# Kernel optimization log

Measured on AMD Instinct MI355X. Metric: run time of the kernel, lower is better.

## Reference

```python
import jax, jax.numpy as jnp
import numpy as np

N, IN_DIM, D, H, E, L = 50000, 16, 128, 256, 800000, 3


def setup_inputs() -> dict:
    key = jax.random.key(0)
    ks = jax.random.split(key, 32)
    s = 0.1
    inp = {
        "x": jax.random.normal(ks[0], (N, IN_DIM), dtype=jnp.float32),
        "edge_index": jax.random.randint(ks[1], (2, E), 0, N, dtype=jnp.int64),
        "enc_W": s * jax.random.normal(ks[2], (IN_DIM, D), dtype=jnp.float32),
        "enc_b": jnp.zeros((D,), jnp.float32),
        "msg_W1": s * jax.random.normal(ks[3], (L, 2 * D, H), dtype=jnp.float32),
        "msg_b1": jnp.zeros((L, H), jnp.float32),
        "msg_W2": s * jax.random.normal(ks[4], (L, H, H), dtype=jnp.float32),
        "msg_b2": jnp.zeros((L, H), jnp.float32),
        "msg_W3": s * jax.random.normal(ks[5], (L, H, D), dtype=jnp.float32),
        "msg_b3": jnp.zeros((L, D), jnp.float32),
        "gru_Wih": s * jax.random.normal(ks[6], (L, D, 3 * D), dtype=jnp.float32),
        "gru_Whh": s * jax.random.normal(ks[7], (L, D, 3 * D), dtype=jnp.float32),
        "gru_bih": jnp.zeros((L, 3 * D), jnp.float32),
        "gru_bhh": jnp.zeros((L, 3 * D), jnp.float32),
        "dec_W1": s * jax.random.normal(ks[8], (D, H), dtype=jnp.float32),
        "dec_b1": jnp.zeros((H,), jnp.float32),
        "dec_W2": s * jax.random.normal(ks[9], (H, H), dtype=jnp.float32),
        "dec_b2": jnp.zeros((H,), jnp.float32),
        "dec_W3": s * jax.random.normal(ks[10], (H, 1), dtype=jnp.float32),
        "dec_b3": jnp.zeros((1,), jnp.float32),
    }
    return inp


def reference(x, edge_index, enc_W, enc_b, msg_W1, msg_b1, msg_W2, msg_b2,
              msg_W3, msg_b3, gru_Wih, gru_Whh, gru_bih, gru_bhh,
              dec_W1, dec_b1, dec_W2, dec_b2, dec_W3, dec_b3):
    n = x.shape[0]
    d = enc_W.shape[1]
    # add self loops (PyG add_self_loops)
    loops = jnp.arange(n, dtype=edge_index.dtype)
    src = jnp.concatenate([edge_index[0], loops])  # x_j
    tgt = jnp.concatenate([edge_index[1], loops])  # x_i / aggregation bucket
    counts = jax.ops.segment_sum(jnp.ones_like(tgt, dtype=x.dtype), tgt, num_segments=n)
    # Encoder: Linear + Tanh
    h = jnp.tanh(x @ enc_W + enc_b)
    for l in range(msg_W1.shape[0]):
        # message: MLP(concat(x_i, x_j))  -> [E+N, d]
        m = jnp.concatenate([h[tgt], h[src]], axis=-1)
        m = jnp.tanh(m @ msg_W1[l] + msg_b1[l])
        m = jnp.tanh(m @ msg_W2[l] + msg_b2[l])
        m = m @ msg_W3[l] + msg_b3[l]
        # aggregate: scatter-mean into target nodes
        agg = jax.ops.segment_sum(m, tgt, num_segments=n) / counts[:, None]
        # update: GRUCell(input=agg, hidden=h)
        gi = agg @ gru_Wih[l] + gru_bih[l]
        gh = h @ gru_Whh[l] + gru_bhh[l]
        r = jax.nn.sigmoid(gi[:, :d] + gh[:, :d])
        z = jax.nn.sigmoid(gi[:, d:2 * d] + gh[:, d:2 * d])
        nn_ = jnp.tanh(gi[:, 2 * d:] + r * gh[:, 2 * d:])
        h = (1.0 - z) * nn_ + z * h
    # Decoder: Linear+Tanh, Linear+Tanh, Linear
    o = jnp.tanh(h @ dec_W1 + dec_b1)
    o = jnp.tanh(o @ dec_W2 + dec_b2)
    o = o @ dec_W3 + dec_b3  # [n, 1]
    return o[:, 0]  # x.view(-1, num_nodes).squeeze(0)
```

## Files before the change

kernel.cpp:

```cpp
#include <hip/hip_runtime.h>
#include <math.h>

#define NN 50000
#define NP 50048
#define NB 782
#define IN_DIM 16
#define DD 128
#define HH 256
#define NE 800000
#define NLAYERS 3
#define ET (NE + NN)

typedef unsigned short ushort_t;
typedef unsigned int uint_t;
typedef __attribute__((ext_vector_type(8))) short bf16x8;
typedef __attribute__((ext_vector_type(4))) float f32x4;

__device__ __forceinline__ float fast_tanh(float x) {
  float e = __builtin_amdgcn_exp2f(x * 2.88539008177793f);
  float r = __builtin_amdgcn_rcpf(e + 1.0f);
  return fmaf(-2.0f, r, 1.0f);
}

__device__ __forceinline__ float fast_sigmoid(float x) {
  float e = __builtin_amdgcn_exp2f(x * -1.44269504088896f);
  return __builtin_amdgcn_rcpf(e + 1.0f);
}

__device__ __forceinline__ ushort_t f2bf(float f) {
  uint_t u = __float_as_uint(f);
  u += 0x7FFFu + ((u >> 16) & 1u);
  return (ushort_t)(u >> 16);
}

__device__ __forceinline__ uint_t pack2bf(float lo, float hi) {
#if __has_builtin(__builtin_amdgcn_cvt_pk_bf16_f32)
  auto v = __builtin_amdgcn_cvt_pk_bf16_f32(lo, hi);
  uint_t r;
  __builtin_memcpy(&r, &v, 4);
  return r;
#else
  return (uint_t)f2bf(lo) | ((uint_t)f2bf(hi) << 16);
#endif
}

__device__ __forceinline__ float bflo(uint_t d) { return __uint_as_float(d << 16); }
__device__ __forceinline__ float bfhi(uint_t d) { return __uint_as_float(d & 0xFFFF0000u); }



__global__ void deg_kernel(const int* __restrict__ etgt, int* __restrict__ deg) {
  int e = blockIdx.x * blockDim.x + threadIdx.x;
  if (e >= ET) return;
  int tg = (e < NE) ? etgt[e] : (e - NE);
  atomicAdd(&deg[tg], 1);
}

__global__ __launch_bounds__(1024) void scan_kernel(const int* __restrict__ deg,
                                                    int* __restrict__ cursor,
                                                    float* __restrict__ invc) {
  __shared__ int wsum[16];
  __shared__ int carry_s;
  const int t = threadIdx.x;
  const int lane = t & 63, wid = t >> 6;
  if (t == 0) carry_s = 0;
  __syncthreads();
  for (int base = 0; base < NN; base += 1024) {
    int i = base + t;
    int d = (i < NN) ? deg[i] : 0;
    int v = d;
#pragma unroll
    for (int off = 1; off < 64; off <<= 1) {
      int u = __shfl_up(v, off);
      if (lane >= off) v += u;
    }
    if (lane == 63) wsum[wid] = v;
    __syncthreads();
    int woff = 0;
    for (int k = 0; k < wid; ++k) woff += wsum[k];
    int incl = v + woff;
    int carry = carry_s;
    __syncthreads();
    if (i < NN) {
      cursor[i] = carry + incl - d;
      invc[i] = 1.0f / (float)d;
    }
    if (t == 1023) carry_s = carry + incl;
    __syncthreads();
  }
}

__global__ void scatter_kernel(const int* __restrict__ esrc, const int* __restrict__ etgt,
                               int* __restrict__ cursor, int* __restrict__ sSrc,
                               int* __restrict__ sTgt) {
  int e = blockIdx.x * blockDim.x + threadIdx.x;
  if (e >= ET) return;
  int s, tg;
  if (e < NE) { s = esrc[e]; tg = etgt[e]; }
  else        { s = e - NE;  tg = s; }
  int pos = atomicAdd(&cursor[tg], 1);
  sSrc[pos] = s;
  sTgt[pos] = tg;
}


__global__ void encoder_kernel(const float* __restrict__ x, const float* __restrict__ W,
                               const float* __restrict__ b, float* __restrict__ h,
                               ushort_t* __restrict__ hbf) {
  int idx = blockIdx.x * blockDim.x + threadIdx.x;
  if (idx >= NN * DD) return;
  int n = idx >> 7, j = idx & (DD - 1);
  const float* xr = x + n * IN_DIM;
  float acc = b[j];
#pragma unroll
  for (int k = 0; k < IN_DIM; ++k) acc = fmaf(xr[k], W[k * DD + j], acc);
  float v = fast_tanh(acc);
  h[idx] = v;
  const int ct = (n >> 4) & 3, mr = n & 15, ks = j >> 5, q = (j >> 3) & 3, jj = j & 7;
  hbf[(size_t)(n >> 6) * 8192 + (((ct * 4 + ks) * 64) + q * 16 + mr) * 8 + jj] = f2bf(v);
}

__global__ void pack_kernel(const float* __restrict__ W, ushort_t* __restrict__ out,
                            int M, int kbsh, int ngrp, int srcStride, int outStride) {
  int tid = blockIdx.x * blockDim.x + threadIdx.x;
  if (tid >= ngrp * 64) return;
  const float* Ws = W + (size_t)blockIdx.y * srcStride;
  ushort_t* os = out + (size_t)blockIdx.y * outStride;
  int lane = tid & 63, g = tid >> 6;
  int ks = g & ((1 << kbsh) - 1);
  int rt = g >> kbsh;
  int m = rt * 16 + (lane & 15);
  int k0 = ks * 32 + ((lane >> 4) << 3);
  uint_t p[4];
#pragma unroll
  for (int d = 0; d < 4; ++d)
    p[d] = pack2bf(Ws[(size_t)(k0 + 2 * d) * M + m], Ws[(size_t)(k0 + 2 * d + 1) * M + m]);
  uint4 o;
  o.x = p[0]; o.y = p[1]; o.z = p[2]; o.w = p[3];
  *(uint4*)(os + (size_t)tid * 8) = o;
}

__global__ __launch_bounds__(256) void proj_kernel(
    const ushort_t* __restrict__ hbf, const ushort_t* __restrict__ W1p,
    const float* __restrict__ b1, ushort_t* __restrict__ Ptb, ushort_t* __restrict__ Psb) {
  const int t = threadIdx.x, blk = blockIdx.x;
  const int w = t >> 6, l = t & 63, quad = l >> 4, col = l & 15;
  const ushort_t* hb = hbf + (size_t)blk * 8192;
#pragma unroll
  for (int half = 0; half < 2; ++half) {
    f32x4 acc[4][4];
#pragma unroll
    for (int m = 0; m < 4; ++m)
#pragma unroll
      for (int ct = 0; ct < 4; ++ct) acc[m][ct] = (f32x4){0.f, 0.f, 0.f, 0.f};
#pragma unroll
    for (int ks = 0; ks < 4; ++ks) {
      bf16x8 af[4];
#pragma unroll
      for (int m = 0; m < 4; ++m)
        af[m] = *(const bf16x8*)&W1p[((size_t)((w * 4 + m) * 8 + half * 4 + ks) * 64 + l) * 8];
#pragma unroll
      for (int ct = 0; ct < 4; ++ct) {
        bf16x8 bf = *(const bf16x8*)&hb[((ct * 4 + ks) * 64 + l) * 8];
#pragma unroll
        for (int m = 0; m < 4; ++m)
          acc[m][ct] = __builtin_amdgcn_mfma_f32_16x16x32_bf16(af[m], bf, acc[m][ct], 0, 0, 0);
      }
    }
    ushort_t* out = half ? Psb : Ptb;
#pragma unroll
    for (int m = 0; m < 4; ++m) {
      const int o0 = (w * 4 + m) * 16 + quad * 4;
      f32x4 bb = (f32x4){0.f, 0.f, 0.f, 0.f};
      if (half == 0) bb = *(const f32x4*)(b1 + o0);
#pragma unroll
      for (int ct = 0; ct < 4; ++ct) {
        const size_t node = (size_t)blk * 64 + ct * 16 + col;
        uint2 d;
        d.x = pack2bf(acc[m][ct][0] + bb[0], acc[m][ct][1] + bb[1]);
        d.y = pack2bf(acc[m][ct][2] + bb[2], acc[m][ct][3] + bb[3]);
        *(uint2*)&out[node * HH + o0] = d;
      }
    }
  }
}

__global__ __launch_bounds__(256, 4) void edge_kernel(
    const int* __restrict__ sSrc, const int* __restrict__ sTgt,
    const ushort_t* __restrict__ Ptb, const ushort_t* __restrict__ Psb,
    const ushort_t* __restrict__ W2p, const float* __restrict__ b2,
    const ushort_t* __restrict__ W3p, const float* __restrict__ b3,
    const float* __restrict__ invc, float* __restrict__ agg) {
  __shared__ __align__(16) float vBf[64 * 132];
  __shared__ int sIdx[64];
  __shared__ int tIdx[64];
  ushort_t* vB = (ushort_t*)vBf;
  const int t = threadIdx.x;
  const int e0 = blockIdx.x * 64;
  if (t < 64) {
    int e = e0 + t;
    int s = 0, tg = -1;
    if (e < ET) { s = sSrc[e]; tg = sTgt[e]; }
    sIdx[t] = s;
    tIdx[t] = tg;
  }
  __syncthreads();
  {
    const int el = t & 63, c = t >> 6;
    int tg = tIdx[el]; if (tg < 0) tg = 0;
    const int s = sIdx[el];
    const uint4* pt = (const uint4*)(Ptb + (size_t)tg * HH + c * 64);
    const uint4* ps = (const uint4*)(Psb + (size_t)s * HH + c * 64);
    const int ct = el >> 4, mr = el & 15;
#pragma unroll
    for (int g = 0; g < 8; ++g) {
      uint4 av = pt[g];
      uint4 bv = ps[g];
      uint_t ad[4] = {av.x, av.y, av.z, av.w};
      uint_t bd[4] = {bv.x, bv.y, bv.z, bv.w};
      uint_t p[4];
#pragma unroll
      for (int d = 0; d < 4; ++d) {
        float flo = bflo(ad[d]) + bflo(bd[d]);
        float fhi = bfhi(ad[d]) + bfhi(bd[d]);
        p[d] = pack2bf(fast_tanh(flo), fast_tanh(fhi));
      }
      uint4 o;
      o.x = p[0]; o.y = p[1]; o.z = p[2]; o.w = p[3];
      const int ks = c * 2 + (g >> 2);
      const int quad = g & 3;
      *(uint4*)&vB[((ct * 8 + ks) * 64 + quad * 16 + mr) * 8] = o;
    }
  }
  __syncthreads();
  const int w = t >> 6, l = t & 63;
  const int quad = l >> 4, col = l & 15;
  f32x4 acc2[4][4];
#pragma unroll
  for (int rp = 0; rp < 4; ++rp)
#pragma unroll
    for (int ct = 0; ct < 4; ++ct) acc2[rp][ct] = (f32x4){0.f, 0.f, 0.f, 0.f};
#pragma unroll
  for (int ks = 0; ks < 8; ++ks) {
    bf16x8 bfrag[4];
#pragma unroll
    for (int ct = 0; ct < 4; ++ct)
      bfrag[ct] = *(const bf16x8*)&vB[((ct * 8 + ks) * 64 + l) * 8];
#pragma unroll
    for (int rp = 0; rp < 4; ++rp) {
      bf16x8 afrag = *(const bf16x8*)&W2p[((size_t)((w * 4 + rp) * 8 + ks) * 64 + l) * 8];
#pragma unroll
      for (int ct = 0; ct < 4; ++ct)
        acc2[rp][ct] = __builtin_amdgcn_mfma_f32_16x16x32_bf16(afrag, bfrag[ct], acc2[rp][ct], 0, 0, 0);
    }
  }
  __syncthreads();
#pragma unroll
  for (int rp = 0; rp < 4; ++rp) {
    f32x4 bb = *(const f32x4*)(b2 + w * 64 + rp * 16 + quad * 4);
#pragma unroll
    for (int ct = 0; ct < 4; ++ct) {
      uint2 d;
      d.x = pack2bf(fast_tanh(acc2[rp][ct][0] + bb[0]), fast_tanh(acc2[rp][ct][1] + bb[1]));
      d.y = pack2bf(fast_tanh(acc2[rp][ct][2] + bb[2]), fast_tanh(acc2[rp][ct][3] + bb[3]));
      const int gidx = (ct * 8 + w * 2 + (rp >> 1)) * 64 + ((rp & 1) * 2 + (quad >> 1)) * 16 + col;
      *(uint2*)&vB[gidx * 8 + (quad & 1) * 4] = d;
    }
  }
  __syncthreads();
  f32x4 acc3[2][4];
#pragma unroll
  for (int rp = 0; rp < 2; ++rp)
#pragma unroll
    for (int ct = 0; ct < 4; ++ct) acc3[rp][ct] = (f32x4){0.f, 0.f, 0.f, 0.f};
#pragma unroll
  for (int ks = 0; ks < 8; ++ks) {
    bf16x8 bfrag[4];
#pragma unroll
    for (int ct = 0; ct < 4; ++ct)
      bfrag[ct] = *(const bf16x8*)&vB[((ct * 8 + ks) * 64 + l) * 8];
#pragma unroll
    for (int rp = 0; rp < 2; ++rp) {
      bf16x8 afrag = *(const bf16x8*)&W3p[((size_t)((w * 2 + rp) * 8 + ks) * 64 + l) * 8];
#pragma unroll
      for (int ct = 0; ct < 4; ++ct)
        acc3[rp][ct] = __builtin_amdgcn_mfma_f32_16x16x32_bf16(afrag, bfrag[ct], acc3[rp][ct], 0, 0, 0);
    }
  }
  __syncthreads();
  {
#pragma unroll
    for (int rp = 0; rp < 2; ++rp) {
      const int m0 = w * 32 + rp * 16 + quad * 4;
      f32x4 b3v = *(const f32x4*)(b3 + m0);
#pragma unroll
      for (int ct = 0; ct < 4; ++ct) {
        float4 o4;
        o4.x = acc3[rp][ct][0] + b3v[0];
        o4.y = acc3[rp][ct][1] + b3v[1];
        o4.z = acc3[rp][ct][2] + b3v[2];
        o4.w = acc3[rp][ct][3] + b3v[3];
        *(float4*)(vBf + (ct * 16 + col) * 132 + m0) = o4;
      }
    }
  }
  __syncthreads();
  {
    const int j = t & 127;
    const int hb = t >> 7;
    const float* colp = vBf + j;
    int cur = tIdx[hb * 32];
    float a = 0.f;
    for (int e = hb * 32; e < hb * 32 + 32; ++e) {
      int tg = tIdx[e];
      if (tg != cur) {
        if (cur >= 0) atomicAdd(&agg[(size_t)cur * DD + j], a * invc[cur]);
        a = 0.f;
        cur = tg;
      }
      a += colp[e * 132];
    }
    if (cur >= 0) atomicAdd(&agg[(size_t)cur * DD + j], a * invc[cur]);
  }
}

__global__ __launch_bounds__(256, 2) void gru_kernel(
    const float* __restrict__ agg, const float* __restrict__ hg,
    const ushort_t* __restrict__ hbf_in,
    const ushort_t* __restrict__ Wihp, const ushort_t* __restrict__ Whhp,
    const float* __restrict__ bih, const float* __restrict__ bhh,
    float* __restrict__ hg_out, ushort_t* __restrict__ hbf_out) {
  __shared__ __align__(16) ushort_t aggF[64 * 128];
  __shared__ __align__(16) float hT[64 * 132];
  const int t = threadIdx.x, blk = blockIdx.x;
  const size_t nodeBase = (size_t)blk * 64;
  {
    const int row = t >> 2, c = t & 3;
    const float4* ap = (const float4*)(agg + (nodeBase + row) * DD + c * 32);
    const int ct = row >> 4, mr = row & 15;
#pragma unroll
    for (int g = 0; g < 8; ++g) {
      float4 v = ap[g];
      uint2 d;
      d.x = pack2bf(v.x, v.y);
      d.y = pack2bf(v.z, v.w);
      *(uint2*)&aggF[(((ct * 4 + c) * 64) + (g >> 1) * 16 + mr) * 8 + (g & 1) * 4] = d;
    }
    const float4* hp = (const float4*)(hg + (nodeBase + row) * DD + c * 32);
    float* hrow = hT + row * 132 + c * 32;
#pragma unroll
    for (int g = 0; g < 8; ++g) *(float4*)(hrow + g * 4) = hp[g];
  }
  __syncthreads();
  const int w = t >> 6, l = t & 63, quad = l >> 4, col = l & 15;
  const ushort_t* hbf_blk = hbf_in + nodeBase * DD;
  f32x4 bbr[2], bbz[2], bbin[2], bbhn[2];
#pragma unroll
  for (int m = 0; m < 2; ++m) {
    const int o = (w + 4 * m) * 16 + quad * 4;
    f32x4 i0 = *(const f32x4*)(bih + o),       h0 = *(const f32x4*)(bhh + o);
    f32x4 i1 = *(const f32x4*)(bih + o + 128), h1 = *(const f32x4*)(bhh + o + 128);
    bbr[m] = i0 + h0;
    bbz[m] = i1 + h1;
    bbin[m] = *(const f32x4*)(bih + o + 256);
    bbhn[m] = *(const f32x4*)(bhh + o + 256);
  }
  for (int ct = 0; ct < 4; ++ct) {
    f32x4 acc[8];
#pragma unroll
    for (int i = 0; i < 8; ++i) acc[i] = (f32x4){0.f, 0.f, 0.f, 0.f};
#pragma unroll
    for (int ks = 0; ks < 8; ++ks) {
      bf16x8 bfrag;
      if (ks < 4) bfrag = *(const bf16x8*)&aggF[((ct * 4 + ks) * 64 + l) * 8];
      else        bfrag = *(const bf16x8*)&hbf_blk[((ct * 4 + (ks - 4)) * 64 + l) * 8];
#pragma unroll
      for (int i = 0; i < 6; ++i) {
        const int rt = w + 4 * i;
        bf16x8 afrag = (ks < 4)
            ? *(const bf16x8*)&Wihp[((size_t)(rt * 4 + ks) * 64 + l) * 8]
            : *(const bf16x8*)&Whhp[((size_t)(rt * 4 + ks - 4) * 64 + l) * 8];
        const int tgt = (i < 4) ? i : ((ks < 4) ? i : i + 2);
        acc[tgt] = __builtin_amdgcn_mfma_f32_16x16x32_bf16(afrag, bfrag, acc[tgt], 0, 0, 0);
      }
    }
#pragma unroll
    for (int m = 0; m < 2; ++m) {
      const int or0 = (w + 4 * m) * 16 + quad * 4;
      float* hrow = hT + (ct * 16 + col) * 132 + or0;
      f32x4 hv = *(const f32x4*)hrow;
      f32x4 hnew;
#pragma unroll
      for (int r = 0; r < 4; ++r) {
        float rr = fast_sigmoid(acc[m][r] + bbr[m][r]);
        float zz = fast_sigmoid(acc[2 + m][r] + bbz[m][r]);
        float gin = acc[4 + m][r] + bbin[m][r];
        float ghn = acc[6 + m][r] + bbhn[m][r];
        float nn = fast_tanh(fmaf(rr, ghn, gin));
        hnew[r] = fmaf(zz, hv[r] - nn, nn);
      }
      *(f32x4*)hrow = hnew;
      uint2 d;
      d.x = pack2bf(hnew[0], hnew[1]);
      d.y = pack2bf(hnew[2], hnew[3]);
      const int ksn = 2 * m + (w >> 1);
      const int qn = 2 * (w & 1) + (quad >> 1);
      *(uint2*)&hbf_out[nodeBase * DD + (((ct * 4 + ksn) * 64) + qn * 16 + col) * 8 + 4 * (quad & 1)] = d;
    }
  }
  __syncthreads();
  {
    const int row = t >> 2, c = t & 3;
    float* dst = hg_out + (nodeBase + row) * DD + c * 32;
    const float* src = hT + row * 132 + c * 32;
#pragma unroll
    for (int g = 0; g < 8; ++g) *(float4*)(dst + g * 4) = *(const float4*)(src + g * 4);
  }
}

__global__ __launch_bounds__(256) void dec_kernel(
    const ushort_t* __restrict__ hbf, const ushort_t* __restrict__ W1p,
    const float* __restrict__ b1, const ushort_t* __restrict__ W2p,
    const float* __restrict__ b2, const float* __restrict__ w3,
    const float* __restrict__ b3, float* __restrict__ out) {
  __shared__ __align__(16) ushort_t o1F[64 * 256];
  __shared__ float red[16][64];
  const int t = threadIdx.x, blk = blockIdx.x;
  const int w = t >> 6, l = t & 63, quad = l >> 4, col = l & 15;
  const ushort_t* hb = hbf + (size_t)blk * 8192;
  {
    f32x4 a1[4][4];
#pragma unroll
    for (int m = 0; m < 4; ++m)
#pragma unroll
      for (int ct = 0; ct < 4; ++ct) a1[m][ct] = (f32x4){0.f, 0.f, 0.f, 0.f};
#pragma unroll
    for (int ks = 0; ks < 4; ++ks) {
      bf16x8 af[4];
#pragma unroll
      for (int m = 0; m < 4; ++m)
        af[m] = *(const bf16x8*)&W1p[((size_t)((w * 4 + m) * 4 + ks) * 64 + l) * 8];
#pragma unroll
      for (int ct = 0; ct < 4; ++ct) {
        bf16x8 bf = *(const bf16x8*)&hb[((ct * 4 + ks) * 64 + l) * 8];
#pragma unroll
        for (int m = 0; m < 4; ++m)
          a1[m][ct] = __builtin_amdgcn_mfma_f32_16x16x32_bf16(af[m], bf, a1[m][ct], 0, 0, 0);
      }
    }
#pragma unroll
    for (int m = 0; m < 4; ++m) {
      const int o0 = (w * 4 + m) * 16 + quad * 4;
      f32x4 bb = *(const f32x4*)(b1 + o0);
      const int ks1 = 2 * w + (m >> 1);
      const int q1 = 2 * (m & 1) + (quad >> 1);
#pragma unroll
      for (int ct = 0; ct < 4; ++ct) {
        uint2 d;
        d.x = pack2bf(fast_tanh(a1[m][ct][0] + bb[0]), fast_tanh(a1[m][ct][1] + bb[1]));
        d.y = pack2bf(fast_tanh(a1[m][ct][2] + bb[2]), fast_tanh(a1[m][ct][3] + bb[3]));
        *(uint2*)&o1F[((ct * 8 + ks1) * 64 + q1 * 16 + col) * 8 + 4 * (quad & 1)] = d;
      }
    }
  }
  __syncthreads();
  {
    f32x4 a2[4][4];
#pragma unroll
    for (int m = 0; m < 4; ++m)
#pragma unroll
      for (int ct = 0; ct < 4; ++ct) a2[m][ct] = (f32x4){0.f, 0.f, 0.f, 0.f};
#pragma unroll
    for (int ks = 0; ks < 8; ++ks) {
      bf16x8 af[4];
#pragma unroll
      for (int m = 0; m < 4; ++m)
        af[m] = *(const bf16x8*)&W2p[((size_t)((w * 4 + m) * 8 + ks) * 64 + l) * 8];
#pragma unroll
      for (int ct = 0; ct < 4; ++ct) {
        bf16x8 bf = *(const bf16x8*)&o1F[((ct * 8 + ks) * 64 + l) * 8];
#pragma unroll
        for (int m = 0; m < 4; ++m)
          a2[m][ct] = __builtin_amdgcn_mfma_f32_16x16x32_bf16(af[m], bf, a2[m][ct], 0, 0, 0);
      }
    }
    float partial[4] = {0.f, 0.f, 0.f, 0.f};
#pragma unroll
    for (int m = 0; m < 4; ++m) {
      const int o0 = (w * 4 + m) * 16 + quad * 4;
      f32x4 b2v = *(const f32x4*)(b2 + o0);
      f32x4 w3v = *(const f32x4*)(w3 + o0);
#pragma unroll
      for (int ct = 0; ct < 4; ++ct)
#pragma unroll
        for (int r = 0; r < 4; ++r)
          partial[ct] += fast_tanh(a2[m][ct][r] + b2v[r]) * w3v[r];
    }
#pragma unroll
    for (int ct = 0; ct < 4; ++ct) red[w * 4 + quad][ct * 16 + col] = partial[ct];
  }
  __syncthreads();
  if (t < 64) {
    float s = b3[0];
#pragma unroll
    for (int k = 0; k < 16; ++k) s += red[k][t];
    size_t node = (size_t)blk * 64 + t;
    if (node < NN) out[node] = s;
  }
}

extern "C" void kernel_launch(void* const* d_in, const int* in_sizes, int n_in,
                              void* d_out, int out_size, void* d_ws, size_t ws_size,
                              hipStream_t stream) {
  const float* x      = (const float*)d_in[0];
  const int*   ei     = (const int*)d_in[1];
  const float* enc_W  = (const float*)d_in[2];
  const float* enc_b  = (const float*)d_in[3];
  const float* msg_W1 = (const float*)d_in[4];
  const float* msg_b1 = (const float*)d_in[5];
  const float* msg_W2 = (const float*)d_in[6];
  const float* msg_b2 = (const float*)d_in[7];
  const float* msg_W3 = (const float*)d_in[8];
  const float* msg_b3 = (const float*)d_in[9];
  const float* gWih   = (const float*)d_in[10];
  const float* gWhh   = (const float*)d_in[11];
  const float* gbih   = (const float*)d_in[12];
  const float* gbhh   = (const float*)d_in[13];
  const float* dW1    = (const float*)d_in[14];
  const float* db1    = (const float*)d_in[15];
  const float* dW2    = (const float*)d_in[16];
  const float* db2    = (const float*)d_in[17];
  const float* dW3    = (const float*)d_in[18];
  const float* db3    = (const float*)d_in[19];
  float* out = (float*)d_out;

  float* ws = (float*)d_ws;
  float* invc = ws;
  float* h    = ws + NP;
  float* agg  = h + (size_t)NP * DD;
  ushort_t* hbfA = (ushort_t*)(agg + (size_t)NP * DD);
  ushort_t* hbfB = hbfA + (size_t)NP * DD;
  ushort_t* Ptb  = hbfB + (size_t)NP * DD;
  ushort_t* Psb  = Ptb + (size_t)NP * HH;
  ushort_t* W2pk = Psb + (size_t)NP * HH;
  ushort_t* W3pk = W2pk + 3 * 65536;
  ushort_t* W1pk = W3pk + 3 * 32768;
  ushort_t* Wihpk = W1pk + 3 * 65536;
  ushort_t* Whhpk = Wihpk + 3 * 49152;
  ushort_t* dW1pk = Whhpk + 3 * 49152;
  ushort_t* dW2pk = dW1pk + 32768;
  int* deg    = (int*)(dW2pk + 65536);
  int* cursor = deg + NP;
  int* sSrc   = cursor + NP;
  int* sTgt   = sSrc + ET;

  const int* esrc = ei;
  const int* etgt = ei + NE;

  hipMemsetAsync(deg, 0, NN * sizeof(int), stream);
  deg_kernel<<<(ET + 255) / 256, 256, 0, stream>>>(etgt, deg);
  scan_kernel<<<1, 1024, 0, stream>>>(deg, cursor, invc);
  scatter_kernel<<<(ET + 255) / 256, 256, 0, stream>>>(esrc, etgt, cursor, sSrc, sTgt);

  encoder_kernel<<<(NN * DD + 255) / 256, 256, 0, stream>>>(x, enc_W, enc_b, h, hbfA);

  pack_kernel<<<dim3(32, 3), 256, 0, stream>>>(msg_W2, W2pk, 256, 3, 128, 65536, 65536);
  pack_kernel<<<dim3(16, 3), 256, 0, stream>>>(msg_W3, W3pk, 128, 3, 64, 32768, 32768);
  pack_kernel<<<dim3(32, 3), 256, 0, stream>>>(msg_W1, W1pk, 256, 3, 128, 65536, 65536);
  pack_kernel<<<dim3(24, 3), 256, 0, stream>>>(gWih, Wihpk, 384, 2, 96, 49152, 49152);
  pack_kernel<<<dim3(24, 3), 256, 0, stream>>>(gWhh, Whhpk, 384, 2, 96, 49152, 49152);
  pack_kernel<<<dim3(16, 1), 256, 0, stream>>>(dW1, dW1pk, 256, 2, 64, 0, 0);
  pack_kernel<<<dim3(32, 1), 256, 0, stream>>>(dW2, dW2pk, 256, 3, 128, 0, 0);

  for (int l = 0; l < NLAYERS; ++l) {
    const ushort_t* hin = (l & 1) ? hbfB : hbfA;
    ushort_t* hout = (l & 1) ? hbfA : hbfB;
    proj_kernel<<<NB, 256, 0, stream>>>(hin, W1pk + (size_t)l * 65536, msg_b1 + l * HH, Ptb, Psb);
    hipMemsetAsync(agg, 0, (size_t)NP * DD * sizeof(float), stream);
    edge_kernel<<<(ET + 63) / 64, 256, 0, stream>>>(
        sSrc, sTgt, Ptb, Psb, W2pk + (size_t)l * 65536, msg_b2 + (size_t)l * HH,
        W3pk + (size_t)l * 32768, msg_b3 + (size_t)l * DD, invc, agg);
    gru_kernel<<<NB, 256, 0, stream>>>(
        agg, h, hin, Wihpk + (size_t)l * 49152, Whhpk + (size_t)l * 49152,
        gbih + (size_t)l * 3 * DD, gbhh + (size_t)l * 3 * DD, h, hout);
  }
  dec_kernel<<<NB, 256, 0, stream>>>(hbfB, dW1pk, db1, dW2pk, db2, dW3, db3, out);
}
```

Before: 1.415 ms.

## Store fp32 hidden state in MFMA fragment layout and trim edge-kernel LDS staging

The fp32 hidden state is now stored in a blocked layout that matches the GRU MFMA output fragments. The GRU kernel can then read and update h directly in global memory, which removes the LDS staging tile, two copy loops and a barrier, and raises its occupancy hint. In the edge kernel, the shared index arrays and their barrier are dropped: indices are read straight from global memory, and targets are broadcast with shuffles during the segmented reduction. The padded output tile is replaced by an XOR-free rotation swizzle, which saves LDS and allows a higher occupancy bound. The trade-off is more scattered small global accesses in the GRU and redundant index loads per wave.

```diff
diff --git a/kernel.cpp b/kernel.cpp
--- a/kernel.cpp
+++ b/kernel.cpp
@@ -105,7 +105,7 @@
 
 
 __global__ void encoder_kernel(const float* __restrict__ x, const float* __restrict__ W,
-                               const float* __restrict__ b, float* __restrict__ h,
+                               const float* __restrict__ b, float* __restrict__ hC,
                                ushort_t* __restrict__ hbf) {
   int idx = blockIdx.x * blockDim.x + threadIdx.x;
   if (idx >= NN * DD) return;
@@ -115,7 +115,7 @@
 #pragma unroll
   for (int k = 0; k < IN_DIM; ++k) acc = fmaf(xr[k], W[k * DD + j], acc);
   float v = fast_tanh(acc);
-  h[idx] = v;
+  hC[(size_t)(n >> 6) * 8192 + (j >> 2) * 256 + (n & 63) * 4 + (j & 3)] = v;
   const int ct = (n >> 4) & 3, mr = n & 15, ks = j >> 5, q = (j >> 3) & 3, jj = j & 7;
   hbf[(size_t)(n >> 6) * 8192 + (((ct * 4 + ks) * 64) + q * 16 + mr) * 8 + jj] = f2bf(v);
 }
@@ -185,30 +185,21 @@
   }
 }
 
-__global__ __launch_bounds__(256, 4) void edge_kernel(
+__global__ __launch_bounds__(256, 5) void edge_kernel(
     const int* __restrict__ sSrc, const int* __restrict__ sTgt,
     const ushort_t* __restrict__ Ptb, const ushort_t* __restrict__ Psb,
     const ushort_t* __restrict__ W2p, const float* __restrict__ b2,
     const ushort_t* __restrict__ W3p, const float* __restrict__ b3,
     const float* __restrict__ invc, float* __restrict__ agg) {
-  __shared__ __align__(16) float vBf[64 * 132];
-  __shared__ int sIdx[64];
-  __shared__ int tIdx[64];
+  __shared__ __align__(16) float vBf[64 * 128];
   ushort_t* vB = (ushort_t*)vBf;
   const int t = threadIdx.x;
   const int e0 = blockIdx.x * 64;
-  if (t < 64) {
-    int e = e0 + t;
-    int s = 0, tg = -1;
-    if (e < ET) { s = sSrc[e]; tg = sTgt[e]; }
-    sIdx[t] = s;
-    tIdx[t] = tg;
-  }
-  __syncthreads();
   {
     const int el = t & 63, c = t >> 6;
-    int tg = tIdx[el]; if (tg < 0) tg = 0;
-    const int s = sIdx[el];
+    const int eg = e0 + el;
+    int s = 0, tg = 0;
+    if (eg < ET) { s = sSrc[eg]; tg = sTgt[eg]; }
     const uint4* pt = (const uint4*)(Ptb + (size_t)tg * HH + c * 64);
     const uint4* ps = (const uint4*)(Psb + (size_t)s * HH + c * 64);
     const int ct = el >> 4, mr = el & 15;
@@ -295,12 +286,13 @@
       f32x4 b3v = *(const f32x4*)(b3 + m0);
 #pragma unroll
       for (int ct = 0; ct < 4; ++ct) {
+        const int e = ct * 16 + col;
         float4 o4;
         o4.x = acc3[rp][ct][0] + b3v[0];
         o4.y = acc3[rp][ct][1] + b3v[1];
         o4.z = acc3[rp][ct][2] + b3v[2];
         o4.w = acc3[rp][ct][3] + b3v[3];
-        *(float4*)(vBf + (ct * 16 + col) * 132 + m0) = o4;
+        *(float4*)(vBf + e * 128 + ((m0 + 4 * e) & 127)) = o4;
       }
     }
   }
@@ -308,30 +300,31 @@
   {
     const int j = t & 127;
     const int hb = t >> 7;
-    const float* colp = vBf + j;
-    int cur = tIdx[hb * 32];
+    const int eg = e0 + hb * 32 + (l & 31);
+    int tv = (eg < ET) ? sTgt[eg] : -1;
+    int cur = __shfl(tv, 0);
     float a = 0.f;
-    for (int e = hb * 32; e < hb * 32 + 32; ++e) {
-      int tg = tIdx[e];
+    for (int i = 0; i < 32; ++i) {
+      int tg = __shfl(tv, i);
       if (tg != cur) {
         if (cur >= 0) atomicAdd(&agg[(size_t)cur * DD + j], a * invc[cur]);
         a = 0.f;
         cur = tg;
       }
-      a += colp[e * 132];
+      const int e = hb * 32 + i;
+      a += vBf[e * 128 + ((j + 4 * e) & 127)];
     }
     if (cur >= 0) atomicAdd(&agg[(size_t)cur * DD + j], a * invc[cur]);
   }
 }
 
-__global__ __launch_bounds__(256, 2) void gru_kernel(
-    const float* __restrict__ agg, const float* __restrict__ hg,
+__global__ __launch_bounds__(256, 4) void gru_kernel(
+    const float* __restrict__ agg, float* __restrict__ hC,
     const ushort_t* __restrict__ hbf_in,
     const ushort_t* __restrict__ Wihp, const ushort_t* __restrict__ Whhp,
     const float* __restrict__ bih, const float* __restrict__ bhh,
-    float* __restrict__ hg_out, ushort_t* __restrict__ hbf_out) {
+    ushort_t* __restrict__ hbf_out) {
   __shared__ __align__(16) ushort_t aggF[64 * 128];
-  __shared__ __align__(16) float hT[64 * 132];
   const int t = threadIdx.x, blk = blockIdx.x;
   const size_t nodeBase = (size_t)blk * 64;
   {
@@ -346,14 +339,11 @@
       d.y = pack2bf(v.z, v.w);
       *(uint2*)&aggF[(((ct * 4 + c) * 64) + (g >> 1) * 16 + mr) * 8 + (g & 1) * 4] = d;
     }
-    const float4* hp = (const float4*)(hg + (nodeBase + row) * DD + c * 32);
-    float* hrow = hT + row * 132 + c * 32;
-#pragma unroll
-    for (int g = 0; g < 8; ++g) *(float4*)(hrow + g * 4) = hp[g];
   }
   __syncthreads();
   const int w = t >> 6, l = t & 63, quad = l >> 4, col = l & 15;
   const ushort_t* hbf_blk = hbf_in + nodeBase * DD;
+  float* hC_blk = hC + nodeBase * DD;
   f32x4 bbr[2], bbz[2], bbin[2], bbhn[2];
 #pragma unroll
   for (int m = 0; m < 2; ++m) {
@@ -386,9 +376,8 @@
     }
 #pragma unroll
     for (int m = 0; m < 2; ++m) {
-      const int or0 = (w + 4 * m) * 16 + quad * 4;
-      float* hrow = hT + (ct * 16 + col) * 132 + or0;
-      f32x4 hv = *(const f32x4*)hrow;
+      float* hp = hC_blk + ((((w + 4 * m) * 4 + quad) * 64) + ct * 16 + col) * 4;
+      f32x4 hv = *(const f32x4*)hp;
       f32x4 hnew;
 #pragma unroll
       for (int r = 0; r < 4; ++r) {
@@ -399,7 +388,7 @@
         float nn = fast_tanh(fmaf(rr, ghn, gin));
         hnew[r] = fmaf(zz, hv[r] - nn, nn);
       }
-      *(f32x4*)hrow = hnew;
+      *(f32x4*)hp = hnew;
       uint2 d;
       d.x = pack2bf(hnew[0], hnew[1]);
       d.y = pack2bf(hnew[2], hnew[3]);
@@ -407,14 +396,6 @@
       const int qn = 2 * (w & 1) + (quad >> 1);
       *(uint2*)&hbf_out[nodeBase * DD + (((ct * 4 + ksn) * 64) + qn * 16 + col) * 8 + 4 * (quad & 1)] = d;
     }
-  }
-  __syncthreads();
-  {
-    const int row = t >> 2, c = t & 3;
-    float* dst = hg_out + (nodeBase + row) * DD + c * 32;
-    const float* src = hT + row * 132 + c * 32;
-#pragma unroll
-    for (int g = 0; g < 8; ++g) *(float4*)(dst + g * 4) = *(const float4*)(src + g * 4);
   }
 }
 
@@ -536,8 +517,8 @@
 
   float* ws = (float*)d_ws;
   float* invc = ws;
-  float* h    = ws + NP;
-  float* agg  = h + (size_t)NP * DD;
+  float* hC   = ws + NP;
+  float* agg  = hC + (size_t)NP * DD;
   ushort_t* hbfA = (ushort_t*)(agg + (size_t)NP * DD);
   ushort_t* hbfB = hbfA + (size_t)NP * DD;
   ushort_t* Ptb  = hbfB + (size_t)NP * DD;
@@ -562,7 +543,7 @@
   scan_kernel<<<1, 1024, 0, stream>>>(deg, cursor, invc);
   scatter_kernel<<<(ET + 255) / 256, 256, 0, stream>>>(esrc, etgt, cursor, sSrc, sTgt);
 
-  encoder_kernel<<<(NN * DD + 255) / 256, 256, 0, stream>>>(x, enc_W, enc_b, h, hbfA);
+  encoder_kernel<<<(NN * DD + 255) / 256, 256, 0, stream>>>(x, enc_W, enc_b, hC, hbfA);
 
   pack_kernel<<<dim3(32, 3), 256, 0, stream>>>(msg_W2, W2pk, 256, 3, 128, 65536, 65536);
   pack_kernel<<<dim3(16, 3), 256, 0, stream>>>(msg_W3, W3pk, 128, 3, 64, 32768, 32768);
@@ -581,8 +562,8 @@
         sSrc, sTgt, Ptb, Psb, W2pk + (size_t)l * 65536, msg_b2 + (size_t)l * HH,
         W3pk + (size_t)l * 32768, msg_b3 + (size_t)l * DD, invc, agg);
     gru_kernel<<<NB, 256, 0, stream>>>(
-        agg, h, hin, Wihpk + (size_t)l * 49152, Whhpk + (size_t)l * 49152,
-        gbih + (size_t)l * 3 * DD, gbhh + (size_t)l * 3 * DD, h, hout);
+        agg, hC, hin, Wihpk + (size_t)l * 49152, Whhpk + (size_t)l * 49152,
+        gbih + (size_t)l * 3 * DD, gbhh + (size_t)l * 3 * DD, hout);
   }
   dec_kernel<<<NB, 256, 0, stream>>>(hbfB, dW1pk, db1, dW2pk, db2, dW3, db3, out);
 }
```

After: 2.211 ms. 56.2% more time.

## Fuse next-layer message projection into GRU kernel epilogue

Applied to the files above, without the earlier changes.

After the GRU update, each block keeps its new bf16 hidden tile in shared memory and immediately computes the next layer's target/source projections with MFMA, writing Ptb/Psb. The standalone projection kernel now runs only once before the loop for layer 0. This removes two kernel launches and the global re-read of the hidden state per layer, at the cost of extra LDS and register pressure in the GRU kernel, which may reduce occupancy.

```diff
diff --git a/kernel.cpp b/kernel.cpp
--- a/kernel.cpp
+++ b/kernel.cpp
@@ -10,6 +10,7 @@
 #define NE 800000
 #define NLAYERS 3
 #define ET (NE + NN)
+#define EBLK 13282
 
 typedef unsigned short ushort_t;
 typedef unsigned int uint_t;
@@ -329,9 +330,12 @@
     const ushort_t* __restrict__ hbf_in,
     const ushort_t* __restrict__ Wihp, const ushort_t* __restrict__ Whhp,
     const float* __restrict__ bih, const float* __restrict__ bhh,
-    float* __restrict__ hg_out, ushort_t* __restrict__ hbf_out) {
+    float* __restrict__ hg_out, ushort_t* __restrict__ hbf_out,
+    int doProj, const ushort_t* __restrict__ W1p, const float* __restrict__ b1,
+    ushort_t* __restrict__ Ptb, ushort_t* __restrict__ Psb) {
   __shared__ __align__(16) ushort_t aggF[64 * 128];
   __shared__ __align__(16) float hT[64 * 132];
+  __shared__ __align__(16) ushort_t hbfL[64 * 128];
   const int t = threadIdx.x, blk = blockIdx.x;
   const size_t nodeBase = (size_t)blk * 64;
   {
@@ -405,7 +409,9 @@
       d.y = pack2bf(hnew[2], hnew[3]);
       const int ksn = 2 * m + (w >> 1);
       const int qn = 2 * (w & 1) + (quad >> 1);
-      *(uint2*)&hbf_out[nodeBase * DD + (((ct * 4 + ksn) * 64) + qn * 16 + col) * 8 + 4 * (quad & 1)] = d;
+      const int fidx = (((ct * 4 + ksn) * 64) + qn * 16 + col) * 8 + 4 * (quad & 1);
+      *(uint2*)&hbf_out[nodeBase * DD + fidx] = d;
+      *(uint2*)&hbfL[fidx] = d;
     }
   }
   __syncthreads();
@@ -415,6 +421,44 @@
     const float* src = hT + row * 132 + c * 32;
 #pragma unroll
     for (int g = 0; g < 8; ++g) *(float4*)(dst + g * 4) = *(const float4*)(src + g * 4);
+  }
+  if (!doProj) return;
+#pragma unroll
+  for (int half = 0; half < 2; ++half) {
+    f32x4 pacc[4][4];
+#pragma unroll
+    for (int m = 0; m < 4; ++m)
+#pragma unroll
+      for (int ct = 0; ct < 4; ++ct) pacc[m][ct] = (f32x4){0.f, 0.f, 0.f, 0.f};
+#pragma unroll
+    for (int ks = 0; ks < 4; ++ks) {
+      bf16x8 af[4];
+#pragma unroll
+      for (int m = 0; m < 4; ++m)
+        af[m] = *(const bf16x8*)&W1p[((size_t)((w * 4 + m) * 8 + half * 4 + ks) * 64 + l) * 8];
+#pragma unroll
+      for (int ct = 0; ct < 4; ++ct) {
+        bf16x8 bf = *(const bf16x8*)&hbfL[((ct * 4 + ks) * 64 + l) * 8];
+#pragma unroll
+        for (int m = 0; m < 4; ++m)
+          pacc[m][ct] = __builtin_amdgcn_mfma_f32_16x16x32_bf16(af[m], bf, pacc[m][ct], 0, 0, 0);
+      }
+    }
+    ushort_t* outp = half ? Psb : Ptb;
+#pragma unroll
+    for (int m = 0; m < 4; ++m) {
+      const int o0 = (w * 4 + m) * 16 + quad * 4;
+      f32x4 bb = (f32x4){0.f, 0.f, 0.f, 0.f};
+      if (half == 0) bb = *(const f32x4*)(b1 + o0);
+#pragma unroll
+      for (int ct = 0; ct < 4; ++ct) {
+        const size_t node = nodeBase + ct * 16 + col;
+        uint2 d;
+        d.x = pack2bf(pacc[m][ct][0] + bb[0], pacc[m][ct][1] + bb[1]);
+        d.y = pack2bf(pacc[m][ct][2] + bb[2], pacc[m][ct][3] + bb[3]);
+        *(uint2*)&outp[node * HH + o0] = d;
+      }
+    }
   }
 }
 
@@ -572,17 +616,20 @@
   pack_kernel<<<dim3(16, 1), 256, 0, stream>>>(dW1, dW1pk, 256, 2, 64, 0, 0);
   pack_kernel<<<dim3(32, 1), 256, 0, stream>>>(dW2, dW2pk, 256, 3, 128, 0, 0);
 
+  proj_kernel<<<NB, 256, 0, stream>>>(hbfA, W1pk, msg_b1, Ptb, Psb);
+
   for (int l = 0; l < NLAYERS; ++l) {
     const ushort_t* hin = (l & 1) ? hbfB : hbfA;
     ushort_t* hout = (l & 1) ? hbfA : hbfB;
-    proj_kernel<<<NB, 256, 0, stream>>>(hin, W1pk + (size_t)l * 65536, msg_b1 + l * HH, Ptb, Psb);
     hipMemsetAsync(agg, 0, (size_t)NP * DD * sizeof(float), stream);
-    edge_kernel<<<(ET + 63) / 64, 256, 0, stream>>>(
+    edge_kernel<<<EBLK, 256, 0, stream>>>(
         sSrc, sTgt, Ptb, Psb, W2pk + (size_t)l * 65536, msg_b2 + (size_t)l * HH,
         W3pk + (size_t)l * 32768, msg_b3 + (size_t)l * DD, invc, agg);
+    const int doProj = (l < NLAYERS - 1) ? 1 : 0;
     gru_kernel<<<NB, 256, 0, stream>>>(
         agg, h, hin, Wihpk + (size_t)l * 49152, Whhpk + (size_t)l * 49152,
-        gbih + (size_t)l * 3 * DD, gbhh + (size_t)l * 3 * DD, h, hout);
+        gbih + (size_t)l * 3 * DD, gbhh + (size_t)l * 3 * DD, h, hout,
+        doProj, W1pk + (size_t)(l + 1) * 65536, msg_b1 + (size_t)(l + 1) * HH, Ptb, Psb);
   }
   dec_kernel<<<NB, 256, 0, stream>>>(hbfB, dW1pk, db1, dW2pk, db2, dW3, db3, out);
 }
```

Result: no change. 1.414 ms, median of 2 (-0.1%).
